# Kernel optimization log

Hardware: AMD Instinct MI355X
Metric: run time of the kernel (lower is better)

The kernel has to match this reference:

```python
import jax, jax.numpy as jnp
import numpy as np

EMBED = 1024
HEADS = 16
HEAD_DIM = EMBED // HEADS
LN_EPS = 1e-5


def _layer_norm(x, g, b):
    m = jnp.mean(x, axis=-1, keepdims=True)
    v = jnp.mean((x - m) ** 2, axis=-1, keepdims=True)
    return (x - m) / jnp.sqrt(v + LN_EPS) * g + b


def _rope(x):
    # x: (b, H, n, D); standard rotary: freqs repeated (cat(freqs, freqs)), rotate_half
    D = x.shape[-1]
    n = x.shape[2]
    inv_freq = 1.0 / (10000.0 ** (jnp.arange(0, D, 2, dtype=jnp.float32) / D))
    freqs = jnp.arange(n, dtype=jnp.float32)[:, None] * inv_freq[None, :]  # (n, D/2)
    emb = jnp.concatenate([freqs, freqs], axis=-1)  # (n, D)
    cos, sin = jnp.cos(emb), jnp.sin(emb)
    rot = jnp.concatenate([-x[..., D // 2:], x[..., : D // 2]], axis=-1)
    return x * cos + rot * sin


def setup_inputs() -> dict:
    key = jax.random.key(0)
    ks = jax.random.split(key, 8)
    E = EMBED
    s_in = 1.0 / np.sqrt(E)
    return {
        "x": jax.random.normal(ks[0], (2, 2048, E), dtype=jnp.float32),
        "in_proj_w": jax.random.uniform(ks[1], (3 * E, E), jnp.float32, -s_in, s_in),
        "in_proj_b": jnp.zeros((3 * E,), jnp.float32),
        "out_proj_w": jax.random.uniform(ks[2], (E, E), jnp.float32, -s_in, s_in),
        "out_proj_b": jnp.zeros((E,), jnp.float32),
        "geglu_w": jax.random.uniform(ks[3], (2 * E, E), jnp.float32, -s_in, s_in),
        "geglu_b": jnp.zeros((2 * E,), jnp.float32),
        "ln1_g": jnp.ones((E,), jnp.float32),
        "ln1_b": jnp.zeros((E,), jnp.float32),
        "ln2_g": jnp.ones((E,), jnp.float32),
        "ln2_b": jnp.zeros((E,), jnp.float32),
    }


def reference(x, in_proj_w, in_proj_b, out_proj_w, out_proj_b,
              geglu_w, geglu_b, ln1_g, ln1_b, ln2_g, ln2_b):
    b, n, E = x.shape
    H, D = HEADS, HEAD_DIM

    # RoPE applied to raw x (q = k = v = x in the module)
    xh = x.reshape(b, n, H, D).transpose(0, 2, 1, 3)  # (b,H,n,D)
    qr = _rope(xh)
    kr = qr  # q and k are identical pre-projection
    q = qr.transpose(0, 2, 1, 3).reshape(b, n, E)
    k = kr.transpose(0, 2, 1, 3).reshape(b, n, E)
    v = x

    # MultiheadAttention (batch-first semantics): in-proj, per-head SDPA, out-proj
    w_q, w_k, w_v = jnp.split(in_proj_w, 3, axis=0)
    b_q, b_k, b_v = jnp.split(in_proj_b, 3, axis=0)
    qp = (q @ w_q.T + b_q).reshape(b, n, H, D).transpose(0, 2, 1, 3)
    kp = (k @ w_k.T + b_k).reshape(b, n, H, D).transpose(0, 2, 1, 3)
    vp = (v @ w_v.T + b_v).reshape(b, n, H, D).transpose(0, 2, 1, 3)
    scores = jnp.einsum("bhqd,bhkd->bhqk", qp, kp) / jnp.sqrt(jnp.float32(D))
    attn = jax.nn.softmax(scores, axis=-1)
    ctx = jnp.einsum("bhqk,bhkd->bhqd", attn, vp)
    ctx = ctx.transpose(0, 2, 1, 3).reshape(b, n, E)
    attn_out = ctx @ out_proj_w.T + out_proj_b

    # residual + LN1
    h = _layer_norm(x + attn_out, ln1_g, ln1_b)

    # GeGLU: Linear(E -> 2E), chunk, value * gelu(gate) (exact erf gelu like torch)
    proj = h @ geglu_w.T + geglu_b
    val, gate = jnp.split(proj, 2, axis=-1)
    fc_out = val * jax.nn.gelu(gate, approximate=False)

    # residual + LN2
    return _layer_norm(h + fc_out, ln2_g, ln2_b)
```

## Files before the change

kernel.cpp:

```cpp
#include <hip/hip_runtime.h>


typedef __bf16 bf16;
typedef bf16 bf16x8 __attribute__((ext_vector_type(8)));
typedef bf16 bf16x4 __attribute__((ext_vector_type(4)));
typedef float f32x4 __attribute__((ext_vector_type(4)));
typedef float f32x16 __attribute__((ext_vector_type(16)));

#define EMB 1024
#define SEQ 2048
#define NTOK 4096
#define NH 16
#define HD 64

__device__ __forceinline__ f32x4 mfma16(bf16x8 a, bf16x8 b, f32x4 c) {
  return __builtin_amdgcn_mfma_f32_16x16x32_bf16(a, b, c, 0, 0, 0);
}
__device__ __forceinline__ f32x16 mfma32(bf16x8 a, bf16x8 b, f32x16 c) {
  return __builtin_amdgcn_mfma_f32_32x32x16_bf16(a, b, c, 0, 0, 0);
}

__device__ __forceinline__ void gll16(const void* g, void* l) {
  __builtin_amdgcn_global_load_lds(
      (const __attribute__((address_space(1))) void*)g,
      (__attribute__((address_space(3))) void*)l, 16, 0, 0);
}

__device__ __forceinline__ unsigned pk2(float a, float b) {
  union { bf16 h[2]; unsigned u; } t;
  t.h[0] = (bf16)a; t.h[1] = (bf16)b;
  return t.u;
}

__device__ __forceinline__ void xcd_map(int nx, int nwg, int& bx, int& by) {
  const int lin = blockIdx.y * nx + blockIdx.x;
  const int id = (lin & 7) * (nwg >> 3) + (lin >> 3);
  bx = id % nx;
  by = id / nx;
}

__global__ __launch_bounds__(256) void prep_all(
    const float* __restrict__ x, bf16* __restrict__ xb, bf16* __restrict__ qr,
    const float* __restrict__ w0, const float* __restrict__ w1,
    const float* __restrict__ w2, bf16* __restrict__ o0,
    bf16* __restrict__ o1, bf16* __restrict__ o2) {
  const int bid = blockIdx.x;
  if (bid < 8192) {
    int idx = bid * 256 + threadIdx.x;
    int row = idx >> 9;
    int i = idx & 511;
    int h = i >> 5, d2 = i & 31;
    int pos = row & (SEQ - 1);
    int c0 = h * HD + d2;
    size_t base = (size_t)row * EMB;
    float x0 = x[base + c0], x1 = x[base + c0 + 32];
    float invf = exp2f(-(float)d2 * 0.4152410118609203f);
    float ang = (float)pos * invf;
    float sn, cs;
    sincosf(ang, &sn, &cs);
    qr[base + c0] = (bf16)(x0 * cs - x1 * sn);
    qr[base + c0 + 32] = (bf16)(x1 * cs + x0 * sn);
    xb[base + c0] = (bf16)x0;
    xb[base + c0 + 32] = (bf16)x1;
  } else {
    int i = ((bid - 8192) * 256 + threadIdx.x) * 4;
    const float* s; bf16* d; int off;
    if (i < 3 * 1024 * 1024) { s = w0; d = o0; off = i; }
    else if (i < 4 * 1024 * 1024) { s = w1; d = o1; off = i - 3 * 1024 * 1024; }
    else { s = w2; d = o2; off = i - 4 * 1024 * 1024; }
    float4 f = *(const float4*)(s + off);
    d[off] = (bf16)f.x; d[off + 1] = (bf16)f.y;
    d[off + 2] = (bf16)f.z; d[off + 3] = (bf16)f.w;
  }
}

__global__ __launch_bounds__(256) void gemm_in(
    const bf16* __restrict__ Aq, const bf16* __restrict__ Ax,
    const bf16* __restrict__ W, const float* __restrict__ bias,
    bf16* __restrict__ qb, bf16* __restrict__ kv) {
  __shared__ bf16 As[2][4096];
  __shared__ bf16 Bs[2][4096];
  const int tid = threadIdx.x, lane = tid & 63, wave = tid >> 6;
  const int quad = lane >> 4, l16 = lane & 15;
  int bx, by;
  xcd_map(24, 24 * 32, bx, by);
  const int m0 = by * 128, n0 = bx * 128;
  const bf16* A = (n0 < 2048) ? Aq : Ax;
  const int K = 1024;
  const int wm = (wave >> 1) * 64, wn = (wave & 1) * 64;
  const int srow = wave * 32 + (lane >> 2);
  const int scol = (lane & 3) * 8;
  const bf16* a0 = A + (size_t)(m0 + srow) * K + scol;
  const bf16* a1 = A + (size_t)(m0 + srow + 16) * K + scol;
  const bf16* w0p = W + (size_t)(n0 + srow) * K + scol;
  const bf16* w1p = W + (size_t)(n0 + srow + 16) * K + scol;
  gll16(a0, As[0] + wave * 1024);
  gll16(a1, As[0] + wave * 1024 + 512);
  gll16(w0p, Bs[0] + wave * 1024);
  gll16(w1p, Bs[0] + wave * 1024 + 512);
  f32x4 acc[4][4] = {};
  for (int it = 0; it < 32; ++it) {
    const int cur = it & 1, nxt = cur ^ 1;
    if (it + 1 < 32) {
      const int k1 = (it + 1) * 32;
      gll16(a0 + k1, As[nxt] + wave * 1024);
      gll16(a1 + k1, As[nxt] + wave * 1024 + 512);
      gll16(w0p + k1, Bs[nxt] + wave * 1024);
      gll16(w1p + k1, Bs[nxt] + wave * 1024 + 512);
      asm volatile("s_waitcnt vmcnt(4)" ::: "memory");
    } else {
      asm volatile("s_waitcnt vmcnt(0)" ::: "memory");
    }
    __builtin_amdgcn_s_barrier();
    __builtin_amdgcn_sched_barrier(0);
    bf16x8 af[4], bw[4];
#pragma unroll
    for (int t = 0; t < 4; ++t) {
      af[t] = *(const bf16x8*)(As[cur] + (wm + t * 16 + l16) * 32 + quad * 8);
      bw[t] = *(const bf16x8*)(Bs[cur] + (wn + t * 16 + l16) * 32 + quad * 8);
    }
#pragma unroll
    for (int mt = 0; mt < 4; ++mt)
#pragma unroll
      for (int nt = 0; nt < 4; ++nt)
        acc[mt][nt] = mfma16(af[mt], bw[nt], acc[mt][nt]);
    __builtin_amdgcn_sched_barrier(0);
    __builtin_amdgcn_s_barrier();
  }
  if (n0 < 1024) {
#pragma unroll
    for (int mt = 0; mt < 4; ++mt)
      for (int nt = 0; nt < 4; ++nt) {
        const int n = n0 + wn + nt * 16 + l16;
        const float bv = bias[n];
#pragma unroll
        for (int r = 0; r < 4; ++r) {
          const int m = m0 + wm + mt * 16 + quad * 4 + r;
          qb[(size_t)m * 1024 + n] = (bf16)((acc[mt][nt][r] + bv) * 0.125f);
        }
      }
  } else if (n0 < 2048) {
#pragma unroll
    for (int mt = 0; mt < 4; ++mt)
      for (int nt = 0; nt < 4; ++nt) {
        const int n = n0 + wn + nt * 16 + l16;
        const float bv = bias[n];
        const int kd = n - 1024, hh = kd >> 6, d = kd & 63;
        const int dc = d >> 3, dl = d & 7;
#pragma unroll
        for (int r = 0; r < 4; ++r) {
          const int m = m0 + wm + mt * 16 + quad * 4 + r;
          const int bb = m >> 11, s = m & 2047;
          const int t = s >> 6, kr = s & 63;
          const size_t base = ((size_t)((bb * 16 + hh) * 32 + t)) * 8192;
          kv[base + kr * 64 + ((dc ^ (kr & 7)) << 3) + dl] =
              (bf16)((acc[mt][nt][r] + bv) * 1.4426950408889634f);
        }
      }
  } else {
#pragma unroll
    for (int mt = 0; mt < 4; ++mt)
      for (int nt = 0; nt < 4; ++nt) {
        const int n = n0 + wn + nt * 16 + l16;
        const float bv = bias[n];
        const int vd = n - 2048, hh = vd >> 6, d = vd & 63;
        const int m = m0 + wm + mt * 16 + quad * 4;
        const int bb = m >> 11, s = m & 2047;
        const int t = s >> 6, kt = s & 63;
        const int g = kt >> 4, w = kt & 15;
        const int c = 2 * g + ((w >> 2) & 1);
        const int slot = (w & 8) ? 4 : 0;
        const size_t base = ((size_t)((bb * 16 + hh) * 32 + t)) * 8192 + 4096;
        bf16x4 pkv;
#pragma unroll
        for (int r = 0; r < 4; ++r) pkv[r] = (bf16)(acc[mt][nt][r] + bv);
        *(bf16x4*)(kv + base + d * 64 + ((c ^ (d & 7)) << 3) + slot) = pkv;
      }
  }
}

__global__ __launch_bounds__(256) void gemm_bt(
    const bf16* __restrict__ A, const bf16* __restrict__ W,
    const float* __restrict__ bias,
    float* __restrict__ outF, bf16* __restrict__ outB,
    int M, int N, int K, int nbx) {
  __shared__ bf16 As[2][4096];
  __shared__ bf16 Bs[2][4096];
  const int tid = threadIdx.x, lane = tid & 63, wave = tid >> 6;
  const int quad = lane >> 4, l16 = lane & 15;
  int bx, by;
  xcd_map(nbx, nbx * 32, bx, by);
  const int m0 = by * 128, n0 = bx * 128;
  const int wm = (wave >> 1) * 64, wn = (wave & 1) * 64;
  const int srow = wave * 32 + (lane >> 2);
  const int scol = (lane & 3) * 8;
  const bf16* a0 = A + (size_t)(m0 + srow) * K + scol;
  const bf16* a1 = A + (size_t)(m0 + srow + 16) * K + scol;
  const bf16* w0p = W + (size_t)(n0 + srow) * K + scol;
  const bf16* w1p = W + (size_t)(n0 + srow + 16) * K + scol;
  gll16(a0, As[0] + wave * 1024);
  gll16(a1, As[0] + wave * 1024 + 512);
  gll16(w0p, Bs[0] + wave * 1024);
  gll16(w1p, Bs[0] + wave * 1024 + 512);
  f32x4 acc[4][4] = {};
  const int nit = K >> 5;
  for (int it = 0; it < nit; ++it) {
    const int cur = it & 1, nxt = cur ^ 1;
    if (it + 1 < nit) {
      const int k1 = (it + 1) * 32;
      gll16(a0 + k1, As[nxt] + wave * 1024);
      gll16(a1 + k1, As[nxt] + wave * 1024 + 512);
      gll16(w0p + k1, Bs[nxt] + wave * 1024);
      gll16(w1p + k1, Bs[nxt] + wave * 1024 + 512);
      asm volatile("s_waitcnt vmcnt(4)" ::: "memory");
    } else {
      asm volatile("s_waitcnt vmcnt(0)" ::: "memory");
    }
    __builtin_amdgcn_s_barrier();
    __builtin_amdgcn_sched_barrier(0);
    bf16x8 af[4], bw[4];
#pragma unroll
    for (int t = 0; t < 4; ++t) {
      af[t] = *(const bf16x8*)(As[cur] + (wm + t * 16 + l16) * 32 + quad * 8);
      bw[t] = *(const bf16x8*)(Bs[cur] + (wn + t * 16 + l16) * 32 + quad * 8);
    }
#pragma unroll
    for (int mt = 0; mt < 4; ++mt)
#pragma unroll
      for (int nt = 0; nt < 4; ++nt)
        acc[mt][nt] = mfma16(af[mt], bw[nt], acc[mt][nt]);
    __builtin_amdgcn_sched_barrier(0);
    __builtin_amdgcn_s_barrier();
  }
#pragma unroll
  for (int mt = 0; mt < 4; ++mt)
    for (int nt = 0; nt < 4; ++nt) {
      const int n = n0 + wn + nt * 16 + l16;
      const float bv = bias ? bias[n] : 0.0f;
#pragma unroll
      for (int r = 0; r < 4; ++r) {
        const int m = m0 + wm + mt * 16 + quad * 4 + r;
        const float v = acc[mt][nt][r] + bv;
        if (outF) outF[(size_t)m * N + n] = v;
        if (outB) outB[(size_t)m * N + n] = (bf16)v;
      }
    }
}

__global__ __launch_bounds__(256) void gemm_bt64(
    const bf16* __restrict__ A, const bf16* __restrict__ W,
    const float* __restrict__ bias, float* __restrict__ outF,
    int M, int N, int K) {
  __shared__ bf16 As[2][4096];
  __shared__ bf16 Bs[2][2048];
  const int tid = threadIdx.x, lane = tid & 63, wave = tid >> 6;
  const int quad = lane >> 4, l16 = lane & 15;
  int bx, by;
  xcd_map(16, 16 * 32, bx, by);
  const int m0 = by * 128, n0 = bx * 64;
  const int wm = (wave >> 1) * 64, wn = (wave & 1) * 32;
  const int srow = wave * 32 + (lane >> 2);
  const int srowB = wave * 16 + (lane >> 2);
  const int scol = (lane & 3) * 8;
  const bf16* a0 = A + (size_t)(m0 + srow) * K + scol;
  const bf16* a1 = A + (size_t)(m0 + srow + 16) * K + scol;
  const bf16* w0p = W + (size_t)(n0 + srowB) * K + scol;
  gll16(a0, As[0] + wave * 1024);
  gll16(a1, As[0] + wave * 1024 + 512);
  gll16(w0p, Bs[0] + wave * 512);
  f32x4 acc[4][2] = {};
  const int nit = K >> 5;
  for (int it = 0; it < nit; ++it) {
    const int cur = it & 1, nxt = cur ^ 1;
    if (it + 1 < nit) {
      const int k1 = (it + 1) * 32;
      gll16(a0 + k1, As[nxt] + wave * 1024);
      gll16(a1 + k1, As[nxt] + wave * 1024 + 512);
      gll16(w0p + k1, Bs[nxt] + wave * 512);
      asm volatile("s_waitcnt vmcnt(3)" ::: "memory");
    } else {
      asm volatile("s_waitcnt vmcnt(0)" ::: "memory");
    }
    __builtin_amdgcn_s_barrier();
    __builtin_amdgcn_sched_barrier(0);
    bf16x8 af[4], bw[2];
#pragma unroll
    for (int t = 0; t < 4; ++t)
      af[t] = *(const bf16x8*)(As[cur] + (wm + t * 16 + l16) * 32 + quad * 8);
#pragma unroll
    for (int t = 0; t < 2; ++t)
      bw[t] = *(const bf16x8*)(Bs[cur] + (wn + t * 16 + l16) * 32 + quad * 8);
#pragma unroll
    for (int mt = 0; mt < 4; ++mt)
#pragma unroll
      for (int nt = 0; nt < 2; ++nt)
        acc[mt][nt] = mfma16(af[mt], bw[nt], acc[mt][nt]);
    __builtin_amdgcn_sched_barrier(0);
    __builtin_amdgcn_s_barrier();
  }
#pragma unroll
  for (int mt = 0; mt < 4; ++mt)
    for (int nt = 0; nt < 2; ++nt) {
      const int n = n0 + wn + nt * 16 + l16;
      const float bv = bias[n];
#pragma unroll
      for (int r = 0; r < 4; ++r) {
        const int m = m0 + wm + mt * 16 + quad * 4 + r;
        outF[(size_t)m * N + n] = acc[mt][nt][r] + bv;
      }
    }
}

__global__ __launch_bounds__(256, 2) void attn14(
    const bf16* __restrict__ Q, const bf16* __restrict__ KV,
    bf16* __restrict__ ctx) {
  __shared__ __align__(16) bf16 kvb[2][16384];
  __shared__ float Linv[4][32];
  const int tid = threadIdx.x, lane = tid & 63, wave = tid >> 6;
  const int hi = lane >> 5, l31 = lane & 31, l7 = lane & 7;
  const int bid = blockIdx.x;
  const int hb = (bid & 7) * 4 + ((bid >> 3) & 3);
  const int qt = bid >> 5;
  const int h = hb & 15, b = hb >> 4;

  bf16x8 qf[4];
  {
    const int qrow = qt * 128 + wave * 32 + l31;
    const bf16* qp = Q + (size_t)(b * SEQ + qrow) * 1024 + h * HD + hi * 8;
#pragma unroll
    for (int t = 0; t < 4; ++t) qf[t] = *(const bf16x8*)(qp + t * 16);
  }
  asm volatile("s_waitcnt vmcnt(0)" ::: "memory");

  const int soff = tid * 8;
  const bf16* kvg = KV + ((size_t)(b * NH + h) * 32) * 8192 + soff;
#pragma unroll
  for (int i = 0; i < 8; ++i)
    gll16(kvg + i * 2048, kvb[0] + soff + i * 2048);
#pragma unroll
  for (int i = 0; i < 8; ++i)
    gll16(kvg + 16384 + i * 2048, kvb[1] + soff + i * 2048);

  f32x16 o0 = {}, o1 = {};
  float lpart = 0.0f;
  const f32x16 zf = {};

  for (int t = 0; t < 16; ++t) {
    if (t < 15) asm volatile("s_waitcnt vmcnt(8)" ::: "memory");
    else        asm volatile("s_waitcnt vmcnt(0)" ::: "memory");
    __builtin_amdgcn_s_barrier();
    __builtin_amdgcn_sched_barrier(0);
    const bf16* tb = kvb[t & 1];
#pragma unroll
    for (int half = 0; half < 2; ++half) {
      const bf16* ks = tb + half * 8192;
      const bf16* vs = ks + 4096;
      f32x16 s0, s1;
      __builtin_amdgcn_s_setprio(1);
      {
        const int swc = (hi ^ l7) * 8;
        bf16x8 k0 = *(const bf16x8*)(ks + l31 * 64 + swc);
        bf16x8 k1 = *(const bf16x8*)(ks + (32 + l31) * 64 + swc);
        s0 = mfma32(k0, qf[0], zf);
        s1 = mfma32(k1, qf[0], zf);
      }
#pragma unroll
      for (int tt = 1; tt < 4; ++tt) {
        const int swc = ((tt * 2 + hi) ^ l7) * 8;
        bf16x8 k0 = *(const bf16x8*)(ks + l31 * 64 + swc);
        bf16x8 k1 = *(const bf16x8*)(ks + (32 + l31) * 64 + swc);
        s0 = mfma32(k0, qf[tt], s0);
        s1 = mfma32(k1, qf[tt], s1);
      }
      __builtin_amdgcn_s_setprio(0);
      unsigned u[16];
#pragma unroll
      for (int g = 0; g < 8; ++g) {
        const int base = (g & 3) * 4;
        float e0, e1, e2, e3;
        if (g < 4) {
          e0 = __builtin_amdgcn_exp2f(s0[base]);
          e1 = __builtin_amdgcn_exp2f(s0[base + 1]);
          e2 = __builtin_amdgcn_exp2f(s0[base + 2]);
          e3 = __builtin_amdgcn_exp2f(s0[base + 3]);
        } else {
          e0 = __builtin_amdgcn_exp2f(s1[base]);
          e1 = __builtin_amdgcn_exp2f(s1[base + 1]);
          e2 = __builtin_amdgcn_exp2f(s1[base + 2]);
          e3 = __builtin_amdgcn_exp2f(s1[base + 3]);
        }
        lpart += (e0 + e1) + (e2 + e3);
        u[g * 2] = pk2(e0, e1);
        u[g * 2 + 1] = pk2(e2, e3);
      }
      __builtin_amdgcn_s_setprio(1);
#pragma unroll
      for (int kk = 0; kk < 4; ++kk) {
        union { unsigned w[4]; bf16x8 v; } fw;
        fw.w[0] = u[4 * kk]; fw.w[1] = u[4 * kk + 1];
        fw.w[2] = u[4 * kk + 2]; fw.w[3] = u[4 * kk + 3];
        const int c16 = (2 * kk + hi) ^ l7;
        bf16x8 v0 = *(const bf16x8*)(vs + l31 * 64 + c16 * 8);
        bf16x8 v1 = *(const bf16x8*)(vs + (32 + l31) * 64 + c16 * 8);
        o0 = mfma32(fw.v, v0, o0);
        o1 = mfma32(fw.v, v1, o1);
      }
      __builtin_amdgcn_s_setprio(0);
    }
    __builtin_amdgcn_sched_barrier(0);
    __builtin_amdgcn_s_barrier();
    __builtin_amdgcn_sched_barrier(0);
    if (t + 2 < 16) {
      const bf16* src = kvg + (size_t)(t + 2) * 16384;
      bf16* dst = kvb[t & 1] + soff;
#pragma unroll
      for (int i = 0; i < 8; ++i) gll16(src + i * 2048, dst + i * 2048);
    }
  }
  float ltot = lpart + __shfl_xor(lpart, 32, 64);
  if (lane < 32) Linv[wave][lane] = 1.0f / ltot;
#pragma unroll
  for (int r = 0; r < 16; ++r) {
    const int qloc = (r & 3) + 8 * (r >> 2) + 4 * hi;
    const float inv = Linv[wave][qloc];
    const int qrow = qt * 128 + wave * 32 + qloc;
    bf16* cp = ctx + (size_t)(b * SEQ + qrow) * EMB + h * HD;
    cp[l31] = (bf16)(o0[r] * inv);
    cp[32 + l31] = (bf16)(o1[r] * inv);
  }
}

__global__ __launch_bounds__(256) void ln1_k(
    const float* __restrict__ x, const float* __restrict__ ao,
    const float* __restrict__ g, const float* __restrict__ bta,
    float* __restrict__ hF, bf16* __restrict__ hB) {
  int row = blockIdx.x, tid = threadIdx.x;
  const float* xr = x + (size_t)row * EMB;
  const float* ar = ao + (size_t)row * EMB;
  float v[4], s = 0.0f, s2 = 0.0f;
#pragma unroll
  for (int i = 0; i < 4; ++i) {
    float t = xr[tid + i * 256] + ar[tid + i * 256];
    v[i] = t; s += t; s2 += t * t;
  }
#pragma unroll
  for (int off = 1; off < 64; off <<= 1) {
    s += __shfl_xor(s, off, 64);
    s2 += __shfl_xor(s2, off, 64);
  }
  __shared__ float red[8];
  int wave = tid >> 6, lane = tid & 63;
  if (lane == 0) { red[wave] = s; red[4 + wave] = s2; }
  __syncthreads();
  s = red[0] + red[1] + red[2] + red[3];
  s2 = red[4] + red[5] + red[6] + red[7];
  float mean = s * (1.0f / EMB);
  float var = s2 * (1.0f / EMB) - mean * mean;
  float inv = rsqrtf(var + 1e-5f);
#pragma unroll
  for (int i = 0; i < 4; ++i) {
    int c = tid + i * 256;
    float t = (v[i] - mean) * inv * g[c] + bta[c];
    hF[(size_t)row * EMB + c] = t;
    hB[(size_t)row * EMB + c] = (bf16)t;
  }
}

__global__ __launch_bounds__(256) void geglu_ln2(
    const float* __restrict__ h, const bf16* __restrict__ proj,
    const float* __restrict__ g, const float* __restrict__ bta,
    float* __restrict__ out) {
  int row = blockIdx.x, tid = threadIdx.x;
  const float* hr = h + (size_t)row * EMB;
  const bf16* pr = proj + (size_t)row * 2048;
  float v[4], s = 0.0f, s2 = 0.0f;
#pragma unroll
  for (int i = 0; i < 4; ++i) {
    int c = tid + i * 256;
    float val = (float)pr[c];
    float gate = (float)pr[1024 + c];
    float ge = 0.5f * gate * (1.0f + erff(gate * 0.70710678f));
    float t = hr[c] + val * ge;
    v[i] = t; s += t; s2 += t * t;
  }
#pragma unroll
  for (int off = 1; off < 64; off <<= 1) {
    s += __shfl_xor(s, off, 64);
    s2 += __shfl_xor(s2, off, 64);
  }
  __shared__ float red[8];
  int wave = tid >> 6, lane = tid & 63;
  if (lane == 0) { red[wave] = s; red[4 + wave] = s2; }
  __syncthreads();
  s = red[0] + red[1] + red[2] + red[3];
  s2 = red[4] + red[5] + red[6] + red[7];
  float mean = s * (1.0f / EMB);
  float var = s2 * (1.0f / EMB) - mean * mean;
  float inv = rsqrtf(var + 1e-5f);
#pragma unroll
  for (int i = 0; i < 4; ++i) {
    int c = tid + i * 256;
    out[(size_t)row * EMB + c] = (v[i] - mean) * inv * g[c] + bta[c];
  }
}

extern "C" void kernel_launch(void* const* d_in, const int* in_sizes, int n_in,
                              void* d_out, int out_size, void* d_ws, size_t ws_size,
                              hipStream_t stream) {
  const float* x = (const float*)d_in[0];
  const float* inW = (const float*)d_in[1];
  const float* inB = (const float*)d_in[2];
  const float* outW = (const float*)d_in[3];
  const float* opB = (const float*)d_in[4];
  const float* ggW = (const float*)d_in[5];
  const float* ggB = (const float*)d_in[6];
  const float* g1 = (const float*)d_in[7];
  const float* b1 = (const float*)d_in[8];
  const float* g2 = (const float*)d_in[9];
  const float* b2 = (const float*)d_in[10];
  float* out = (float*)d_out;
  char* ws = (char*)d_ws;
  const size_t MB = 1ull << 20;
  bf16* xb = (bf16*)(ws);
  bf16* hB = (bf16*)(ws);
  bf16* qr = (bf16*)(ws + 8 * MB);
  bf16* ctx = (bf16*)(ws + 8 * MB);
  bf16* wI = (bf16*)(ws + 16 * MB);
  bf16* wO = (bf16*)(ws + 22 * MB);
  bf16* wG = (bf16*)(ws + 24 * MB);
  bf16* qb = (bf16*)(ws + 28 * MB);
  bf16* kv = (bf16*)(ws + 36 * MB);
  bf16* projB = (bf16*)(ws + 28 * MB);
  float* ao = (float*)(ws + 52 * MB);

  prep_all<<<8192 + 6144, 256, 0, stream>>>(x, xb, qr, inW, outW, ggW,
                                            wI, wO, wG);
  gemm_in<<<dim3(24, 32), 256, 0, stream>>>(qr, xb, wI, inB, qb, kv);
  attn14<<<512, 256, 0, stream>>>(qb, kv, ctx);
  gemm_bt64<<<dim3(16, 32), 256, 0, stream>>>(ctx, wO, opB, ao,
                                              NTOK, 1024, 1024);
  ln1_k<<<NTOK, 256, 0, stream>>>(x, ao, g1, b1, ao, hB);
  gemm_bt<<<dim3(16, 32), 256, 0, stream>>>(hB, wG, ggB, nullptr, projB,
                                            NTOK, 2048, 1024, 16);
  geglu_ln2<<<NTOK, 256, 0, stream>>>(ao, projB, g2, b2, out);
}
```

Before: 268.4 us.

## Use 256x128 tiles, 8 waves and 4-stage LDS pipeline in input and GeGLU GEMMs

Reworks the in-projection and GeGLU GEMMs to use 512-thread blocks computing 256x128 tiles. A 4-buffer LDS ring keeps three K-slices in flight, with a single barrier per iteration. s_setprio is raised around the MFMA block. The goal is better latency hiding and reuse of the weight tile across more rows, at the cost of 96KB of LDS per block and half as many blocks.

```diff
diff --git a/kernel.cpp b/kernel.cpp
--- a/kernel.cpp
+++ b/kernel.cpp
@@ -74,68 +74,69 @@
   }
 }
 
-__global__ __launch_bounds__(256) void gemm_in(
+__global__ __launch_bounds__(512, 2) void gemm_in(
     const bf16* __restrict__ Aq, const bf16* __restrict__ Ax,
     const bf16* __restrict__ W, const float* __restrict__ bias,
     bf16* __restrict__ qb, bf16* __restrict__ kv) {
-  __shared__ bf16 As[2][4096];
-  __shared__ bf16 Bs[2][4096];
+  __shared__ bf16 Ab[4][8192];
+  __shared__ bf16 Bb[4][4096];
   const int tid = threadIdx.x, lane = tid & 63, wave = tid >> 6;
   const int quad = lane >> 4, l16 = lane & 15;
+  const int wr = wave >> 1, wc = wave & 1;
   int bx, by;
-  xcd_map(24, 24 * 32, bx, by);
-  const int m0 = by * 128, n0 = bx * 128;
+  xcd_map(24, 384, bx, by);
+  const int m0 = by * 256, n0 = bx * 128;
   const bf16* A = (n0 < 2048) ? Aq : Ax;
   const int K = 1024;
-  const int wm = (wave >> 1) * 64, wn = (wave & 1) * 64;
-  const int srow = wave * 32 + (lane >> 2);
-  const int scol = (lane & 3) * 8;
-  const bf16* a0 = A + (size_t)(m0 + srow) * K + scol;
-  const bf16* a1 = A + (size_t)(m0 + srow + 16) * K + scol;
-  const bf16* w0p = W + (size_t)(n0 + srow) * K + scol;
-  const bf16* w1p = W + (size_t)(n0 + srow + 16) * K + scol;
-  gll16(a0, As[0] + wave * 1024);
-  gll16(a1, As[0] + wave * 1024 + 512);
-  gll16(w0p, Bs[0] + wave * 1024);
-  gll16(w1p, Bs[0] + wave * 1024 + 512);
+  const bf16* sa0 = A + (size_t)(m0 + (tid >> 2)) * K + (tid & 3) * 8;
+  const bf16* sa1 = A + (size_t)(m0 + 128 + (tid >> 2)) * K + (tid & 3) * 8;
+  const bf16* sw0 = W + (size_t)(n0 + (tid >> 2)) * K + (tid & 3) * 8;
+  const int doff = tid * 8;
+#pragma unroll
+  for (int t = 0; t < 3; ++t) {
+    gll16(sa0 + t * 32, Ab[t] + doff);
+    gll16(sa1 + t * 32, Ab[t] + 4096 + doff);
+    gll16(sw0 + t * 32, Bb[t] + doff);
+  }
   f32x4 acc[4][4] = {};
-  for (int it = 0; it < 32; ++it) {
-    const int cur = it & 1, nxt = cur ^ 1;
-    if (it + 1 < 32) {
-      const int k1 = (it + 1) * 32;
-      gll16(a0 + k1, As[nxt] + wave * 1024);
-      gll16(a1 + k1, As[nxt] + wave * 1024 + 512);
-      gll16(w0p + k1, Bs[nxt] + wave * 1024);
-      gll16(w1p + k1, Bs[nxt] + wave * 1024 + 512);
-      asm volatile("s_waitcnt vmcnt(4)" ::: "memory");
-    } else {
-      asm volatile("s_waitcnt vmcnt(0)" ::: "memory");
-    }
+  for (int g = 0; g < 32; ++g) {
+    if (g <= 29) asm volatile("s_waitcnt vmcnt(6)" ::: "memory");
+    else         asm volatile("s_waitcnt vmcnt(0)" ::: "memory");
     __builtin_amdgcn_s_barrier();
     __builtin_amdgcn_sched_barrier(0);
+    if (g + 3 < 32) {
+      const int k1 = (g + 3) * 32;
+      bf16* da = Ab[(g + 3) & 3];
+      bf16* db = Bb[(g + 3) & 3];
+      gll16(sa0 + k1, da + doff);
+      gll16(sa1 + k1, da + 4096 + doff);
+      gll16(sw0 + k1, db + doff);
+    }
+    const bf16* As = Ab[g & 3];
+    const bf16* Bs = Bb[g & 3];
     bf16x8 af[4], bw[4];
 #pragma unroll
     for (int t = 0; t < 4; ++t) {
-      af[t] = *(const bf16x8*)(As[cur] + (wm + t * 16 + l16) * 32 + quad * 8);
-      bw[t] = *(const bf16x8*)(Bs[cur] + (wn + t * 16 + l16) * 32 + quad * 8);
-    }
+      af[t] = *(const bf16x8*)(As + (wr * 64 + t * 16 + l16) * 32 + quad * 8);
+      bw[t] = *(const bf16x8*)(Bs + (wc * 64 + t * 16 + l16) * 32 + quad * 8);
+    }
+    __builtin_amdgcn_s_setprio(1);
 #pragma unroll
     for (int mt = 0; mt < 4; ++mt)
 #pragma unroll
       for (int nt = 0; nt < 4; ++nt)
         acc[mt][nt] = mfma16(af[mt], bw[nt], acc[mt][nt]);
-    __builtin_amdgcn_sched_barrier(0);
-    __builtin_amdgcn_s_barrier();
+    __builtin_amdgcn_s_setprio(0);
   }
   if (n0 < 1024) {
 #pragma unroll
     for (int mt = 0; mt < 4; ++mt)
       for (int nt = 0; nt < 4; ++nt) {
-        const int n = n0 + wn + nt * 16 + l16;
+        const int n = n0 + wc * 64 + nt * 16 + l16;
         const float bv = bias[n];
 #pragma unroll
         for (int r = 0; r < 4; ++r) {
-          const int m = m0 + wm + mt * 16 + quad * 4 + r;
+          const int m = m0 + wr * 64 + mt * 16 + quad * 4 + r;
           qb[(size_t)m * 1024 + n] = (bf16)((acc[mt][nt][r] + bv) * 0.125f);
         }
       }
@@ -143,16 +144,16 @@
 #pragma unroll
     for (int mt = 0; mt < 4; ++mt)
       for (int nt = 0; nt < 4; ++nt) {
-        const int n = n0 + wn + nt * 16 + l16;
+        const int n = n0 + wc * 64 + nt * 16 + l16;
         const float bv = bias[n];
         const int kd = n - 1024, hh = kd >> 6, d = kd & 63;
         const int dc = d >> 3, dl = d & 7;
 #pragma unroll
         for (int r = 0; r < 4; ++r) {
-          const int m = m0 + wm + mt * 16 + quad * 4 + r;
+          const int m = m0 + wr * 64 + mt * 16 + quad * 4 + r;
           const int bb = m >> 11, s = m & 2047;
-          const int t = s >> 6, kr = s & 63;
-          const size_t base = ((size_t)((bb * 16 + hh) * 32 + t)) * 8192;
+          const int tt = s >> 6, kr = s & 63;
+          const size_t base = ((size_t)((bb * 16 + hh) * 32 + tt)) * 8192;
           kv[base + kr * 64 + ((dc ^ (kr & 7)) << 3) + dl] =
               (bf16)((acc[mt][nt][r] + bv) * 1.4426950408889634f);
         }
@@ -161,16 +162,16 @@
 #pragma unroll
     for (int mt = 0; mt < 4; ++mt)
       for (int nt = 0; nt < 4; ++nt) {
-        const int n = n0 + wn + nt * 16 + l16;
+        const int n = n0 + wc * 64 + nt * 16 + l16;
         const float bv = bias[n];
         const int vd = n - 2048, hh = vd >> 6, d = vd & 63;
-        const int m = m0 + wm + mt * 16 + quad * 4;
+        const int m = m0 + wr * 64 + mt * 16 + quad * 4;
         const int bb = m >> 11, s = m & 2047;
-        const int t = s >> 6, kt = s & 63;
-        const int g = kt >> 4, w = kt & 15;
-        const int c = 2 * g + ((w >> 2) & 1);
+        const int tt = s >> 6, kt = s & 63;
+        const int g2 = kt >> 4, w = kt & 15;
+        const int c = 2 * g2 + ((w >> 2) & 1);
         const int slot = (w & 8) ? 4 : 0;
-        const size_t base = ((size_t)((bb * 16 + hh) * 32 + t)) * 8192 + 4096;
+        const size_t base = ((size_t)((bb * 16 + hh) * 32 + tt)) * 8192 + 4096;
         bf16x4 pkv;
 #pragma unroll
         for (int r = 0; r < 4; ++r) pkv[r] = (bf16)(acc[mt][nt][r] + bv);
@@ -179,67 +180,68 @@
   }
 }
 
-__global__ __launch_bounds__(256) void gemm_bt(
+__global__ __launch_bounds__(512, 2) void gemm256(
     const bf16* __restrict__ A, const bf16* __restrict__ W,
     const float* __restrict__ bias,
     float* __restrict__ outF, bf16* __restrict__ outB,
     int M, int N, int K, int nbx) {
-  __shared__ bf16 As[2][4096];
-  __shared__ bf16 Bs[2][4096];
+  __shared__ bf16 Ab[4][8192];
+  __shared__ bf16 Bb[4][4096];
   const int tid = threadIdx.x, lane = tid & 63, wave = tid >> 6;
   const int quad = lane >> 4, l16 = lane & 15;
+  const int wr = wave >> 1, wc = wave & 1;
   int bx, by;
-  xcd_map(nbx, nbx * 32, bx, by);
-  const int m0 = by * 128, n0 = bx * 128;
-  const int wm = (wave >> 1) * 64, wn = (wave & 1) * 64;
-  const int srow = wave * 32 + (lane >> 2);
-  const int scol = (lane & 3) * 8;
-  const bf16* a0 = A + (size_t)(m0 + srow) * K + scol;
-  const bf16* a1 = A + (size_t)(m0 + srow + 16) * K + scol;
-  const bf16* w0p = W + (size_t)(n0 + srow) * K + scol;
-  const bf16* w1p = W + (size_t)(n0 + srow + 16) * K + scol;
-  gll16(a0, As[0] + wave * 1024);
-  gll16(a1, As[0] + wave * 1024 + 512);
-  gll16(w0p, Bs[0] + wave * 1024);
-  gll16(w1p, Bs[0] + wave * 1024 + 512);
+  xcd_map(nbx, nbx * (M >> 8), bx, by);
+  const int m0 = by * 256, n0 = bx * 128;
+  const bf16* sa0 = A + (size_t)(m0 + (tid >> 2)) * K + (tid & 3) * 8;
+  const bf16* sa1 = A + (size_t)(m0 + 128 + (tid >> 2)) * K + (tid & 3) * 8;
+  const bf16* sw0 = W + (size_t)(n0 + (tid >> 2)) * K + (tid & 3) * 8;
+  const int doff = tid * 8;
+  const int nit = K >> 5;
+#pragma unroll
+  for (int t = 0; t < 3; ++t) {
+    gll16(sa0 + t * 32, Ab[t] + doff);
+    gll16(sa1 + t * 32, Ab[t] + 4096 + doff);
+    gll16(sw0 + t * 32, Bb[t] + doff);
+  }
   f32x4 acc[4][4] = {};
-  const int nit = K >> 5;
-  for (int it = 0; it < nit; ++it) {
-    const int cur = it & 1, nxt = cur ^ 1;
-    if (it + 1 < nit) {
-      const int k1 = (it + 1) * 32;
-      gll16(a0 + k1, As[nxt] + wave * 1024);
-      gll16(a1 + k1, As[nxt] + wave * 1024 + 512);
-      gll16(w0p + k1, Bs[nxt] + wave * 1024);
-      gll16(w1p + k1, Bs[nxt] + wave * 1024 + 512);
-      asm volatile("s_waitcnt vmcnt(4)" ::: "memory");
-    } else {
-      asm volatile("s_waitcnt vmcnt(0)" ::: "memory");
-    }
+  for (int g = 0; g < nit; ++g) {
+    if (g <= nit - 3) asm volatile("s_waitcnt vmcnt(6)" ::: "memory");
+    else              asm volatile("s_waitcnt vmcnt(0)" ::: "memory");
     __builtin_amdgcn_s_barrier();
     __builtin_amdgcn_sched_barrier(0);
+    if (g + 3 < nit) {
+      const int k1 = (g + 3) * 32;
+      bf16* da = Ab[(g + 3) & 3];
+      bf16* db = Bb[(g + 3) & 3];
+      gll16(sa0 + k1, da + doff);
+      gll16(sa1 + k1, da + 4096 + doff);
+      gll16(sw0 + k1, db + doff);
+    }
+    const bf16* As = Ab[g & 3];
+    const bf16* Bs = Bb[g & 3];
     bf16x8 af[4], bw[4];
 #pragma unroll
     for (int t = 0; t < 4; ++t) {
-      af[t] = *(const bf16x8*)(As[cur] + (wm + t * 16 + l16) * 32 + quad * 8);
-      bw[t] = *(const bf16x8*)(Bs[cur] + (wn + t * 16 + l16) * 32 + quad * 8);
-    }
+      af[t] = *(const bf16x8*)(As + (wr * 64 + t * 16 + l16) * 32 + quad * 8);
+      bw[t] = *(const bf16x8*)(Bs + (wc * 64 + t * 16 + l16) * 32 + quad * 8);
+    }
+    __builtin_amdgcn_s_setprio(1);
 #pragma unroll
     for (int mt = 0; mt < 4; ++mt)
 #pragma unroll
       for (int nt = 0; nt < 4; ++nt)
         acc[mt][nt] = mfma16(af[mt], bw[nt], acc[mt][nt]);
-    __builtin_amdgcn_sched_barrier(0);
-    __builtin_amdgcn_s_barrier();
+    __builtin_amdgcn_s_setprio(0);
   }
 #pragma unroll
   for (int mt = 0; mt < 4; ++mt)
     for (int nt = 0; nt < 4; ++nt) {
-      const int n = n0 + wn + nt * 16 + l16;
+      const int n = n0 + wc * 64 + nt * 16 + l16;
       const float bv = bias ? bias[n] : 0.0f;
 #pragma unroll
       for (int r = 0; r < 4; ++r) {
-        const int m = m0 + wm + mt * 16 + quad * 4 + r;
+        const int m = m0 + wr * 64 + mt * 16 + quad * 4 + r;
         const float v = acc[mt][nt][r] + bv;
         if (outF) outF[(size_t)m * N + n] = v;
         if (outB) outB[(size_t)m * N + n] = (bf16)v;
@@ -535,12 +537,12 @@
 
   prep_all<<<8192 + 6144, 256, 0, stream>>>(x, xb, qr, inW, outW, ggW,
                                             wI, wO, wG);
-  gemm_in<<<dim3(24, 32), 256, 0, stream>>>(qr, xb, wI, inB, qb, kv);
+  gemm_in<<<dim3(24, 16), 512, 0, stream>>>(qr, xb, wI, inB, qb, kv);
   attn14<<<512, 256, 0, stream>>>(qb, kv, ctx);
   gemm_bt64<<<dim3(16, 32), 256, 0, stream>>>(ctx, wO, opB, ao,
                                               NTOK, 1024, 1024);
   ln1_k<<<NTOK, 256, 0, stream>>>(x, ao, g1, b1, ao, hB);
-  gemm_bt<<<dim3(16, 32), 256, 0, stream>>>(hB, wG, ggB, nullptr, projB,
+  gemm256<<<dim3(16, 16), 512, 0, stream>>>(hB, wG, ggB, nullptr, projB,
                                             NTOK, 2048, 1024, 16);
   geglu_ln2<<<NTOK, 256, 0, stream>>>(ao, projB, g2, b2, out);
 }
```

After: 278.5 us. 1.04x slower.

## Triple-buffer GEMM LDS pipeline with swizzled layout and MFMA priority

Applied to the files above, without the earlier changes.

All three GEMM kernels move from a double-buffered to a three-stage LDS ring. Loads are issued two k-steps ahead, right after a single barrier per iteration, which removes the trailing barrier. The global-to-LDS column offset is XOR-swizzled by row, with matching read offsets, to reduce LDS bank conflicts on the fragment reads. s_setprio raises wave priority around the MFMA block. The cost is 50% more LDS per block, which may lower occupancy. The xcd_map row count in gemm_bt is also generalized to M.

```diff
diff --git a/kernel.cpp b/kernel.cpp
--- a/kernel.cpp
+++ b/kernel.cpp
@@ -78,54 +78,63 @@
     const bf16* __restrict__ Aq, const bf16* __restrict__ Ax,
     const bf16* __restrict__ W, const float* __restrict__ bias,
     bf16* __restrict__ qb, bf16* __restrict__ kv) {
-  __shared__ bf16 As[2][4096];
-  __shared__ bf16 Bs[2][4096];
+  __shared__ bf16 Ab[3][4096];
+  __shared__ bf16 Bb[3][4096];
   const int tid = threadIdx.x, lane = tid & 63, wave = tid >> 6;
   const int quad = lane >> 4, l16 = lane & 15;
   int bx, by;
-  xcd_map(24, 24 * 32, bx, by);
+  xcd_map(24, 768, bx, by);
   const int m0 = by * 128, n0 = bx * 128;
   const bf16* A = (n0 < 2048) ? Aq : Ax;
   const int K = 1024;
   const int wm = (wave >> 1) * 64, wn = (wave & 1) * 64;
   const int srow = wave * 32 + (lane >> 2);
-  const int scol = (lane & 3) * 8;
+  const int scol = ((lane & 3) ^ ((lane >> 2) & 3)) * 8;
   const bf16* a0 = A + (size_t)(m0 + srow) * K + scol;
   const bf16* a1 = A + (size_t)(m0 + srow + 16) * K + scol;
   const bf16* w0p = W + (size_t)(n0 + srow) * K + scol;
   const bf16* w1p = W + (size_t)(n0 + srow + 16) * K + scol;
-  gll16(a0, As[0] + wave * 1024);
-  gll16(a1, As[0] + wave * 1024 + 512);
-  gll16(w0p, Bs[0] + wave * 1024);
-  gll16(w1p, Bs[0] + wave * 1024 + 512);
+  const int sq = (quad ^ (l16 & 3)) * 8;
+#pragma unroll
+  for (int t = 0; t < 2; ++t) {
+    gll16(a0 + t * 32, Ab[t] + wave * 1024);
+    gll16(a1 + t * 32, Ab[t] + wave * 1024 + 512);
+    gll16(w0p + t * 32, Bb[t] + wave * 1024);
+    gll16(w1p + t * 32, Bb[t] + wave * 1024 + 512);
+  }
   f32x4 acc[4][4] = {};
-  for (int it = 0; it < 32; ++it) {
-    const int cur = it & 1, nxt = cur ^ 1;
-    if (it + 1 < 32) {
-      const int k1 = (it + 1) * 32;
-      gll16(a0 + k1, As[nxt] + wave * 1024);
-      gll16(a1 + k1, As[nxt] + wave * 1024 + 512);
-      gll16(w0p + k1, Bs[nxt] + wave * 1024);
-      gll16(w1p + k1, Bs[nxt] + wave * 1024 + 512);
-      asm volatile("s_waitcnt vmcnt(4)" ::: "memory");
-    } else {
-      asm volatile("s_waitcnt vmcnt(0)" ::: "memory");
-    }
+  int rd = 0, wr = 2;
+  for (int g = 0; g < 32; ++g) {
+    if (g < 31) asm volatile("s_waitcnt vmcnt(4)" ::: "memory");
+    else        asm volatile("s_waitcnt vmcnt(0)" ::: "memory");
     __builtin_amdgcn_s_barrier();
     __builtin_amdgcn_sched_barrier(0);
+    if (g + 2 < 32) {
+      const int k1 = (g + 2) * 32;
+      bf16* da = Ab[wr];
+      bf16* db = Bb[wr];
+      gll16(a0 + k1, da + wave * 1024);
+      gll16(a1 + k1, da + wave * 1024 + 512);
+      gll16(w0p + k1, db + wave * 1024);
+      gll16(w1p + k1, db + wave * 1024 + 512);
+    }
+    const bf16* As = Ab[rd];
+    const bf16* Bs = Bb[rd];
     bf16x8 af[4], bw[4];
 #pragma unroll
     for (int t = 0; t < 4; ++t) {
-      af[t] = *(const bf16x8*)(As[cur] + (wm + t * 16 + l16) * 32 + quad * 8);
-      bw[t] = *(const bf16x8*)(Bs[cur] + (wn + t * 16 + l16) * 32 + quad * 8);
-    }
+      af[t] = *(const bf16x8*)(As + (wm + t * 16 + l16) * 32 + sq);
+      bw[t] = *(const bf16x8*)(Bs + (wn + t * 16 + l16) * 32 + sq);
+    }
+    __builtin_amdgcn_s_setprio(1);
 #pragma unroll
     for (int mt = 0; mt < 4; ++mt)
 #pragma unroll
       for (int nt = 0; nt < 4; ++nt)
         acc[mt][nt] = mfma16(af[mt], bw[nt], acc[mt][nt]);
-    __builtin_amdgcn_sched_barrier(0);
-    __builtin_amdgcn_s_barrier();
+    __builtin_amdgcn_s_setprio(0);
+    rd = (rd + 1 == 3) ? 0 : rd + 1;
+    wr = (wr + 1 == 3) ? 0 : wr + 1;
   }
   if (n0 < 1024) {
 #pragma unroll
@@ -167,8 +176,8 @@
         const int m = m0 + wm + mt * 16 + quad * 4;
         const int bb = m >> 11, s = m & 2047;
         const int t = s >> 6, kt = s & 63;
-        const int g = kt >> 4, w = kt & 15;
-        const int c = 2 * g + ((w >> 2) & 1);
+        const int g2 = kt >> 4, w = kt & 15;
+        const int c = 2 * g2 + ((w >> 2) & 1);
         const int slot = (w & 8) ? 4 : 0;
         const size_t base = ((size_t)((bb * 16 + hh) * 32 + t)) * 8192 + 4096;
         bf16x4 pkv;
@@ -184,53 +193,62 @@
     const float* __restrict__ bias,
     float* __restrict__ outF, bf16* __restrict__ outB,
     int M, int N, int K, int nbx) {
-  __shared__ bf16 As[2][4096];
-  __shared__ bf16 Bs[2][4096];
+  __shared__ bf16 Ab[3][4096];
+  __shared__ bf16 Bb[3][4096];
   const int tid = threadIdx.x, lane = tid & 63, wave = tid >> 6;
   const int quad = lane >> 4, l16 = lane & 15;
   int bx, by;
-  xcd_map(nbx, nbx * 32, bx, by);
+  xcd_map(nbx, nbx * (M >> 7), bx, by);
   const int m0 = by * 128, n0 = bx * 128;
   const int wm = (wave >> 1) * 64, wn = (wave & 1) * 64;
   const int srow = wave * 32 + (lane >> 2);
-  const int scol = (lane & 3) * 8;
+  const int scol = ((lane & 3) ^ ((lane >> 2) & 3)) * 8;
   const bf16* a0 = A + (size_t)(m0 + srow) * K + scol;
   const bf16* a1 = A + (size_t)(m0 + srow + 16) * K + scol;
   const bf16* w0p = W + (size_t)(n0 + srow) * K + scol;
   const bf16* w1p = W + (size_t)(n0 + srow + 16) * K + scol;
-  gll16(a0, As[0] + wave * 1024);
-  gll16(a1, As[0] + wave * 1024 + 512);
-  gll16(w0p, Bs[0] + wave * 1024);
-  gll16(w1p, Bs[0] + wave * 1024 + 512);
+  const int sq = (quad ^ (l16 & 3)) * 8;
+  const int nit = K >> 5;
+#pragma unroll
+  for (int t = 0; t < 2; ++t) {
+    gll16(a0 + t * 32, Ab[t] + wave * 1024);
+    gll16(a1 + t * 32, Ab[t] + wave * 1024 + 512);
+    gll16(w0p + t * 32, Bb[t] + wave * 1024);
+    gll16(w1p + t * 32, Bb[t] + wave * 1024 + 512);
+  }
   f32x4 acc[4][4] = {};
-  const int nit = K >> 5;
-  for (int it = 0; it < nit; ++it) {
-    const int cur = it & 1, nxt = cur ^ 1;
-    if (it + 1 < nit) {
-      const int k1 = (it + 1) * 32;
-      gll16(a0 + k1, As[nxt] + wave * 1024);
-      gll16(a1 + k1, As[nxt] + wave * 1024 + 512);
-      gll16(w0p + k1, Bs[nxt] + wave * 1024);
-      gll16(w1p + k1, Bs[nxt] + wave * 1024 + 512);
-      asm volatile("s_waitcnt vmcnt(4)" ::: "memory");
-    } else {
-      asm volatile("s_waitcnt vmcnt(0)" ::: "memory");
-    }
+  int rd = 0, wr = 2;
+  for (int g = 0; g < nit; ++g) {
+    if (g < nit - 1) asm volatile("s_waitcnt vmcnt(4)" ::: "memory");
+    else             asm volatile("s_waitcnt vmcnt(0)" ::: "memory");
     __builtin_amdgcn_s_barrier();
     __builtin_amdgcn_sched_barrier(0);
+    if (g + 2 < nit) {
+      const int k1 = (g + 2) * 32;
+      bf16* da = Ab[wr];
+      bf16* db = Bb[wr];
+      gll16(a0 + k1, da + wave * 1024);
+      gll16(a1 + k1, da + wave * 1024 + 512);
+      gll16(w0p + k1, db + wave * 1024);
+      gll16(w1p + k1, db + wave * 1024 + 512);
+    }
+    const bf16* As = Ab[rd];
+    const bf16* Bs = Bb[rd];
     bf16x8 af[4], bw[4];
 #pragma unroll
     for (int t = 0; t < 4; ++t) {
-      af[t] = *(const bf16x8*)(As[cur] + (wm + t * 16 + l16) * 32 + quad * 8);
-      bw[t] = *(const bf16x8*)(Bs[cur] + (wn + t * 16 + l16) * 32 + quad * 8);
-    }
+      af[t] = *(const bf16x8*)(As + (wm + t * 16 + l16) * 32 + sq);
+      bw[t] = *(const bf16x8*)(Bs + (wn + t * 16 + l16) * 32 + sq);
+    }
+    __builtin_amdgcn_s_setprio(1);
 #pragma unroll
     for (int mt = 0; mt < 4; ++mt)
 #pragma unroll
       for (int nt = 0; nt < 4; ++nt)
         acc[mt][nt] = mfma16(af[mt], bw[nt], acc[mt][nt]);
-    __builtin_amdgcn_sched_barrier(0);
-    __builtin_amdgcn_s_barrier();
+    __builtin_amdgcn_s_setprio(0);
+    rd = (rd + 1 == 3) ? 0 : rd + 1;
+    wr = (wr + 1 == 3) ? 0 : wr + 1;
   }
 #pragma unroll
   for (int mt = 0; mt < 4; ++mt)
@@ -251,8 +269,8 @@
     const bf16* __restrict__ A, const bf16* __restrict__ W,
     const float* __restrict__ bias, float* __restrict__ outF,
     int M, int N, int K) {
-  __shared__ bf16 As[2][4096];
-  __shared__ bf16 Bs[2][2048];
+  __shared__ bf16 Ab[3][4096];
+  __shared__ bf16 Bb[3][2048];
   const int tid = threadIdx.x, lane = tid & 63, wave = tid >> 6;
   const int quad = lane >> 4, l16 = lane & 15;
   int bx, by;
@@ -261,42 +279,49 @@
   const int wm = (wave >> 1) * 64, wn = (wave & 1) * 32;
   const int srow = wave * 32 + (lane >> 2);
   const int srowB = wave * 16 + (lane >> 2);
-  const int scol = (lane & 3) * 8;
+  const int scol = ((lane & 3) ^ ((lane >> 2) & 3)) * 8;
   const bf16* a0 = A + (size_t)(m0 + srow) * K + scol;
   const bf16* a1 = A + (size_t)(m0 + srow + 16) * K + scol;
   const bf16* w0p = W + (size_t)(n0 + srowB) * K + scol;
-  gll16(a0, As[0] + wave * 1024);
-  gll16(a1, As[0] + wave * 1024 + 512);
-  gll16(w0p, Bs[0] + wave * 512);
+  const int sq = (quad ^ (l16 & 3)) * 8;
+  const int nit = K >> 5;
+#pragma unroll
+  for (int t = 0; t < 2; ++t) {
+    gll16(a0 + t * 32, Ab[t] + wave * 1024);
+    gll16(a1 + t * 32, Ab[t] + wave * 1024 + 512);
+    gll16(w0p + t * 32, Bb[t] + wave * 512);
+  }
   f32x4 acc[4][2] = {};
-  const int nit = K >> 5;
-  for (int it = 0; it < nit; ++it) {
-    const int cur = it & 1, nxt = cur ^ 1;
-    if (it + 1 < nit) {
-      const int k1 = (it + 1) * 32;
-      gll16(a0 + k1, As[nxt] + wave * 1024);
-      gll16(a1 + k1, As[nxt] + wave * 1024 + 512);
-      gll16(w0p + k1, Bs[nxt] + wave * 512);
-      asm volatile("s_waitcnt vmcnt(3)" ::: "memory");
-    } else {
-      asm volatile("s_waitcnt vmcnt(0)" ::: "memory");
-    }
+  int rd = 0, wr = 2;
+  for (int g = 0; g < nit; ++g) {
+    if (g < nit - 1) asm volatile("s_waitcnt vmcnt(3)" ::: "memory");
+    else             asm volatile("s_waitcnt vmcnt(0)" ::: "memory");
     __builtin_amdgcn_s_barrier();
     __builtin_amdgcn_sched_barrier(0);
+    if (g + 2 < nit) {
+      const int k1 = (g + 2) * 32;
+      gll16(a0 + k1, Ab[wr] + wave * 1024);
+      gll16(a1 + k1, Ab[wr] + wave * 1024 + 512);
+      gll16(w0p + k1, Bb[wr] + wave * 512);
+    }
+    const bf16* As = Ab[rd];
+    const bf16* Bs = Bb[rd];
     bf16x8 af[4], bw[2];
 #pragma unroll
     for (int t = 0; t < 4; ++t)
-      af[t] = *(const bf16x8*)(As[cur] + (wm + t * 16 + l16) * 32 + quad * 8);
+      af[t] = *(const bf16x8*)(As + (wm + t * 16 + l16) * 32 + sq);
 #pragma unroll
     for (int t = 0; t < 2; ++t)
-      bw[t] = *(const bf16x8*)(Bs[cur] + (wn + t * 16 + l16) * 32 + quad * 8);
+      bw[t] = *(const bf16x8*)(Bs + (wn + t * 16 + l16) * 32 + sq);
+    __builtin_amdgcn_s_setprio(1);
 #pragma unroll
     for (int mt = 0; mt < 4; ++mt)
 #pragma unroll
       for (int nt = 0; nt < 2; ++nt)
         acc[mt][nt] = mfma16(af[mt], bw[nt], acc[mt][nt]);
-    __builtin_amdgcn_sched_barrier(0);
-    __builtin_amdgcn_s_barrier();
+    __builtin_amdgcn_s_setprio(0);
+    rd = (rd + 1 == 3) ? 0 : rd + 1;
+    wr = (wr + 1 == 3) ? 0 : wr + 1;
   }
 #pragma unroll
   for (int mt = 0; mt < 4; ++mt)
```

After: 265.0 us. About the same (-1.3%).
